# Optimization experiments

Measured on AMD Instinct MI355X. Metric: run time of the kernel, lower is better.

Reference implementation:

```python
import jax, jax.numpy as jnp
from jax import lax
import numpy as np

EPS = 1e-6
D_KQ = 256  # per-head q/k dim; softmax scale = sqrt(256) = 16


def layernorm(x, g, b):
    m = jnp.mean(x, axis=-1, keepdims=True)
    v = jnp.var(x, axis=-1, keepdims=True)  # biased, matches torch LayerNorm
    return (x - m) / jnp.sqrt(v + EPS) * g + b


def lrelu(t):
    return jnp.where(t > 0, t, 0.1 * t)


def setup_inputs() -> dict:
    key = jax.random.key(0)
    ks = jax.random.split(key, 10)
    B, C, H, W = 256, 17, 84, 84
    d_model, heads = 512, 4
    hid = D_KQ * heads  # 1024
    out_dim = 256
    s = 0.05
    return {
        "x": jax.random.normal(ks[0], (B, C, H, W), jnp.float32),
        "conv1_w": jax.random.normal(ks[1], (64, C, 8, 8), jnp.float32) * s,
        "conv1_b": jnp.zeros((64,), jnp.float32),
        "conv2_w": jax.random.normal(ks[2], (510, 64, 4, 4), jnp.float32) * s,
        "conv2_b": jnp.zeros((510,), jnp.float32),
        "wq": jax.random.normal(ks[3], (hid, d_model), jnp.float32) * s,
        "wk": jax.random.normal(ks[4], (hid, d_model), jnp.float32) * s,
        "wv": jax.random.normal(ks[5], (hid, d_model), jnp.float32) * s,
        "ln_e_g": jnp.ones((hid,), jnp.float32),
        "ln_e_b": jnp.zeros((hid,), jnp.float32),
        "wo": jax.random.normal(ks[6], (d_model, hid), jnp.float32) * s,
        "ln_g": jnp.ones((d_model,), jnp.float32),
        "ln_b": jnp.zeros((d_model,), jnp.float32),
        "map_w": jax.random.normal(ks[7], (out_dim, d_model), jnp.float32) * s,
        "map_b": jnp.zeros((out_dim,), jnp.float32),
    }


def reference(x, conv1_w, conv1_b, conv2_w, conv2_b, wq, wk, wv,
              ln_e_g, ln_e_b, wo, ln_g, ln_b, map_w, map_b):
    dn = ("NCHW", "OIHW", "NCHW")
    # feature extractor
    y = lax.conv_general_dilated(x, conv1_w, (4, 4), "VALID", dimension_numbers=dn)
    y = lrelu(y + conv1_b[None, :, None, None])
    y = lax.conv_general_dilated(y, conv2_w, (2, 2), "VALID", dimension_numbers=dn)
    y = lrelu(y + conv2_b[None, :, None, None])  # [B,510,H2,W2]
    B, Cc, H2, W2 = y.shape
    N = H2 * W2
    e = jnp.transpose(y.reshape(B, Cc, N), (0, 2, 1))  # [B,N,510]
    # coordinate augmentation: [(i//W)/H, (i%W)/W]
    idx = jnp.arange(N)
    coord = jnp.stack([(idx // W2) / H2, (idx % W2) / W2], axis=-1).astype(e.dtype)
    e = jnp.concatenate([e, jnp.broadcast_to(coord, (B, N, 2))], axis=-1)  # [B,N,512]
    heads = 4
    # projections + per-projection LayerNorm over full hid dim (pre-head-split)
    q = layernorm(e @ wq.T, ln_e_g, ln_e_b).reshape(B, N, heads, D_KQ)
    k = layernorm(e @ wk.T, ln_e_g, ln_e_b).reshape(B, N, heads, D_KQ)
    v = layernorm(e @ wv.T, ln_e_g, ln_e_b).reshape(B, N, heads, D_KQ)
    scores = jnp.einsum("bnhd,bmhd->bhnm", q, k) / jnp.sqrt(jnp.float32(D_KQ))
    w = jax.nn.softmax(scores, axis=-1)
    nv = jnp.einsum("bhnm,bmhd->bnhd", w, v).reshape(B, N, heads * D_KQ)
    out = layernorm(nv @ wo.T + e, ln_g, ln_b)  # residual + LN
    out = jax.nn.relu(out)
    out = jnp.max(out, axis=1)  # maxout over entities -> [B,512]
    return lrelu(out @ map_w.T + map_b)  # mapping -> [B,256]
```

## Files before the change

kernel.cpp:

```cpp
#include <hip/hip_runtime.h>
#include <hip/hip_bf16.h>
#include <math.h>

typedef __hip_bfloat16 bf16;
using f32x4 = __attribute__((ext_vector_type(4))) float;
using s16x8 = __attribute__((ext_vector_type(8))) short;

#define DEV_INLINE __device__ __forceinline__

static constexpr int BB   = 256;
static constexpr int CIN  = 17;
static constexpr int WIN  = 84;
static constexpr int C1   = 64;
static constexpr int W1   = 20;
static constexpr int P1   = W1 * W1;
static constexpr int C2   = 510;
static constexpr int W2   = 9;
static constexpr int NE   = 81;
static constexpr int DM   = 512;
static constexpr int HID  = 1024;
static constexpr int NH   = 4;
static constexpr int DK   = 256;
static constexpr int MR   = BB * NE;
static constexpr int ODIM = 256;
static constexpr int PLANE = WIN * WIN;
static constexpr int QS   = 3 * HID;

DEV_INLINE float lrelu_f(float v) { return v > 0.f ? v : 0.1f * v; }
DEV_INLINE float bf2f(ushort u) { return __uint_as_float((unsigned)u << 16); }
DEV_INLINE short f2bs(float f) { bf16 t = __float2bfloat16(f); return *reinterpret_cast<short*>(&t); }

DEV_INLINE void gll16(const void* g, const void* l) {
    __builtin_amdgcn_global_load_lds(
        (const __attribute__((address_space(1))) unsigned int*)g,
        (__attribute__((address_space(3))) unsigned int*)l, 16, 0, 0);
}
DEV_INLINE f32x4 mfma16(s16x8 a, s16x8 b, f32x4 c) {
    return __builtin_amdgcn_mfma_f32_16x16x32_bf16(a, b, c, 0, 0, 0);
}

__global__ void k_cast4(const float* __restrict__ s, bf16* __restrict__ d, int n4) {
    const int i4 = blockIdx.x * 256 + threadIdx.x;
    if (i4 >= n4) return;
    const size_t i = (size_t)i4 * 4;
    const float4 v = *(const float4*)(s + i);
    short o[4] = { f2bs(v.x), f2bs(v.y), f2bs(v.z), f2bs(v.w) };
    *(ushort4*)(d + i) = *(ushort4*)o;
}
__global__ void k_castw2(const float* __restrict__ s, bf16* __restrict__ d) {
    const int i = blockIdx.x * 256 + threadIdx.x;
    const int n = i >> 10, rem = i & 1023;
    const int khkw = rem >> 6, ic = rem & 63;
    d[i] = (n < C2) ? __float2bfloat16(s[n * 1024 + ic * 16 + khkw])
                    : __float2bfloat16(0.f);
}
__global__ void k_padb2(const float* __restrict__ s, float* __restrict__ d) {
    const int i = blockIdx.x * 256 + threadIdx.x;
    if (i < 512) d[i] = (i < C2) ? s[i] : 0.f;
}
__global__ void k_castqkv(const float* __restrict__ wq, const float* __restrict__ wk,
                          const float* __restrict__ wv, bf16* __restrict__ d) {
    const int i4 = blockIdx.x * 256 + threadIdx.x;
    const size_t i = (size_t)i4 * 4;
    const int n = (int)(i >> 9), c = (int)(i & 511);
    const float* src = (n < 1024) ? wq : (n < 2048) ? wk : wv;
    const int r = n & 1023;
    const float4 v = *(const float4*)(src + (size_t)r * 512 + c);
    short o[4] = { f2bs(v.x), f2bs(v.y), f2bs(v.z), f2bs(v.w) };
    *(ushort4*)(d + i) = *(ushort4*)o;
}

__global__ __launch_bounds__(512, 1) void k_conv1_mfma(const float* __restrict__ x,
        const bf16* __restrict__ w1b, const float* __restrict__ bias,
        bf16* __restrict__ y1t) {
    __shared__ __align__(16) char pl[2][28224];
    const int b = blockIdx.x;
    const int tid = threadIdx.x;
    const int w = tid >> 6, l = tid & 63;
    const int l15 = l & 15, l4 = l >> 4;
    const float* xb = x + (size_t)b * CIN * PLANE;

    int baseA[4], tval[4];
    #pragma unroll
    for (int j = 0; j < 4; ++j) {
        const int t = w + 8 * j; tval[j] = t;
        int p = t * 16 + l15; if (t >= 25) p = 0;
        const int oh = p / 20, ow = p % 20;
        baseA[j] = (oh * 4 + l4) * 336 + ow * 16;
    }
    float bias_r[4];
    #pragma unroll
    for (int nt = 0; nt < 4; ++nt) bias_r[nt] = bias[nt * 16 + l15];

    #pragma unroll
    for (int it = 0; it < 4; ++it) {
        const int g = it * 512 + tid;
        if (g < 1764) gll16(xb + (size_t)g * 4, pl[0] + (size_t)g * 16);
    }
    __syncthreads();

    f32x4 acc[4][4] = {};
    int cur = 0;
    for (int ic = 0; ic < CIN; ++ic) {
        if (ic + 1 < CIN) {
            const float* src = xb + (size_t)(ic + 1) * PLANE;
            #pragma unroll
            for (int it = 0; it < 4; ++it) {
                const int g = it * 512 + tid;
                if (g < 1764) gll16(src + (size_t)g * 4, pl[cur ^ 1] + (size_t)g * 16);
            }
        }
        s16x8 bq[4][2];
        #pragma unroll
        for (int nt = 0; nt < 4; ++nt)
            #pragma unroll
            for (int ks = 0; ks < 2; ++ks)
                bq[nt][ks] = *(const s16x8*)(w1b + (size_t)(nt * 16 + l15) * 1088
                                             + ic * 64 + (ks * 4 + l4) * 8);
        const char* P = pl[cur];
        #pragma unroll
        for (int j = 0; j < 4; ++j) {
            if (tval[j] < 25) {
                #pragma unroll
                for (int ks = 0; ks < 2; ++ks) {
                    const float* fp = (const float*)(P + baseA[j] + ks * 1344);
                    const f32x4 f0 = *(const f32x4*)fp;
                    const f32x4 f1 = *(const f32x4*)(fp + 4);
                    s16x8 af;
                    #pragma unroll
                    for (int jj = 0; jj < 4; ++jj) {
                        af[jj]     = f2bs(f0[jj]);
                        af[jj + 4] = f2bs(f1[jj]);
                    }
                    #pragma unroll
                    for (int nt = 0; nt < 4; ++nt)
                        acc[j][nt] = mfma16(af, bq[nt][ks], acc[j][nt]);
                }
            }
        }
        __syncthreads();
        cur ^= 1;
    }
    #pragma unroll
    for (int j = 0; j < 4; ++j) {
        if (tval[j] < 25) {
            #pragma unroll
            for (int nt = 0; nt < 4; ++nt) {
                #pragma unroll
                for (int q = 0; q < 4; ++q) {
                    const int pix = tval[j] * 16 + l4 * 4 + q;
                    const int oc  = nt * 16 + l15;
                    y1t[((size_t)b * P1 + pix) * 64 + oc] =
                        __float2bfloat16(lrelu_f(acc[j][nt][q] + bias_r[nt]));
                }
            }
        }
    }
}

__global__ __launch_bounds__(256) void k_gemm_conv2(const bf16* __restrict__ A,
        const bf16* __restrict__ B, const float* __restrict__ bias,
        bf16* __restrict__ Cb) {
    __shared__ __align__(16) char Asm[2][128 * 64];
    __shared__ __align__(16) char Bsm[2][128 * 64];
    const int tid = threadIdx.x;
    const int m0 = blockIdx.y * 128, n0 = blockIdx.x * 128;
    const int w = tid >> 6, l = tid & 63;
    const int wm = w >> 1, wn = w & 1;
    const int l15 = l & 15, l4 = l >> 4;
    const int r0 = tid >> 2, p0 = tid & 3;
    const int r1 = 64 + r0;
    const int sw0 = (p0 ^ ((r0 >> 1) & 3)) << 3;
    const int sw1 = (p0 ^ ((r1 >> 1) & 3)) << 3;
    int bimg[2], ohh[2], oww[2];
    #pragma unroll
    for (int it = 0; it < 2; ++it) {
        const int m = m0 + (it ? r1 : r0);
        bimg[it] = m / 81;
        const int n = m - bimg[it] * 81;
        ohh[it] = n / 9; oww[it] = n - ohh[it] * 9;
    }
    auto stage = [&](int buf, int k0) {
        const int khkw = k0 >> 6, icb = k0 & 63;
        const int kh = khkw >> 2, kwv = khkw & 3;
        const int pix0 = (ohh[0] * 2 + kh) * 20 + oww[0] * 2 + kwv;
        const int pix1 = (ohh[1] * 2 + kh) * 20 + oww[1] * 2 + kwv;
        gll16(A + ((size_t)bimg[0] * P1 + pix0) * 64 + icb + sw0, Asm[buf] + tid * 16);
        gll16(A + ((size_t)bimg[1] * P1 + pix1) * 64 + icb + sw1, Asm[buf] + (256 + tid) * 16);
        gll16(B + (size_t)(n0 + r0) * HID + k0 + sw0, Bsm[buf] + tid * 16);
        gll16(B + (size_t)(n0 + r1) * HID + k0 + sw1, Bsm[buf] + (256 + tid) * 16);
    };
    stage(0, 0);
    __syncthreads();
    f32x4 acc[4][4] = {};
    int cur = 0;
    for (int t = 0; t < 32; ++t) {
        if (t < 31) stage(cur ^ 1, (t + 1) * 32);
        s16x8 af[4], bfv[4];
        #pragma unroll
        for (int i = 0; i < 4; ++i) {
            const int ra = wm * 64 + i * 16 + l15;
            af[i]  = *(const s16x8*)(Asm[cur] + ra * 64 + ((l4 ^ ((ra >> 1) & 3)) << 4));
            const int rb = wn * 64 + i * 16 + l15;
            bfv[i] = *(const s16x8*)(Bsm[cur] + rb * 64 + ((l4 ^ ((rb >> 1) & 3)) << 4));
        }
        #pragma unroll
        for (int i = 0; i < 4; ++i)
            #pragma unroll
            for (int j = 0; j < 4; ++j)
                acc[i][j] = mfma16(af[i], bfv[j], acc[i][j]);
        __syncthreads();
        cur ^= 1;
    }
    #pragma unroll
    for (int i = 0; i < 4; ++i) {
        #pragma unroll
        for (int j = 0; j < 4; ++j) {
            const int col = n0 + wn * 64 + j * 16 + l15;
            #pragma unroll
            for (int q = 0; q < 4; ++q) {
                const int row = m0 + wm * 64 + i * 16 + l4 * 4 + q;
                float v = lrelu_f(acc[i][j][q] + bias[col]);
                if (col >= 510) {
                    const int n = row % 81;
                    v = (col == 510) ? (float)(n / 9) * (1.f / 9.f)
                                     : (float)(n % 9) * (1.f / 9.f);
                }
                Cb[(size_t)row * DM + col] = __float2bfloat16(v);
            }
        }
    }
}

template <int RESID>
__global__ __launch_bounds__(256) void k_gemm_stats(const bf16* __restrict__ A,
        const bf16* __restrict__ B, const bf16* __restrict__ resid,
        bf16* __restrict__ Cb, float2* __restrict__ part,
        int K, int ldc, int nPH) {
    __shared__ __align__(16) char Asm[2][16384];
    __shared__ __align__(16) char Bsm[2][16384];
    const int tid = threadIdx.x;
    const int m0 = blockIdx.y * 128, n0 = blockIdx.x * 128;
    const int w = tid >> 6, l = tid & 63;
    const int wm = w >> 1, wn = w & 1;
    const int l15 = l & 15, l4 = l >> 4;

    auto stage = [&](int buf, int k0) {
        #pragma unroll
        for (int it = 0; it < 4; ++it) {
            const int g = it * 256 + tid;
            const int r = g >> 3, p = g & 7;
            const int sw = (p ^ (r & 7)) << 3;
            gll16(A + (size_t)(m0 + r) * K + k0 + sw, Asm[buf] + g * 16);
            gll16(B + (size_t)(n0 + r) * K + k0 + sw, Bsm[buf] + g * 16);
        }
    };
    stage(0, 0);
    __syncthreads();
    f32x4 acc[4][4] = {};
    int cur = 0;
    const int nt = K >> 6;
    for (int t = 0; t < nt; ++t) {
        if (t + 1 < nt) stage(cur ^ 1, (t + 1) * 64);
        #pragma unroll
        for (int kk = 0; kk < 2; ++kk) {
            s16x8 af[4], bfv[4];
            const int pz = kk * 4 + l4;
            #pragma unroll
            for (int i = 0; i < 4; ++i) {
                const int ra = wm * 64 + i * 16 + l15;
                af[i]  = *(const s16x8*)(Asm[cur] + ra * 128 + ((pz ^ (ra & 7)) << 4));
                const int rb = wn * 64 + i * 16 + l15;
                bfv[i] = *(const s16x8*)(Bsm[cur] + rb * 128 + ((pz ^ (rb & 7)) << 4));
            }
            #pragma unroll
            for (int i = 0; i < 4; ++i)
                #pragma unroll
                for (int j = 0; j < 4; ++j)
                    acc[i][j] = mfma16(af[i], bfv[j], acc[i][j]);
        }
        __syncthreads();
        cur ^= 1;
    }
    #pragma unroll
    for (int i = 0; i < 4; ++i) {
        #pragma unroll
        for (int q = 0; q < 4; ++q) {
            const int row = m0 + wm * 64 + i * 16 + l4 * 4 + q;
            if (RESID) {
                const bf16* rr = resid + (size_t)row * ldc;
                #pragma unroll
                for (int j = 0; j < 4; ++j)
                    acc[i][j][q] += bf2f(*(const ushort*)(rr + n0 + wn * 64 + j * 16 + l15));
            }
            float s = 0.f, s2 = 0.f;
            #pragma unroll
            for (int j = 0; j < 4; ++j) {
                const float v = acc[i][j][q];
                s += v; s2 += v * v;
            }
            #pragma unroll
            for (int o = 1; o < 16; o <<= 1) {
                s  += __shfl_xor(s, o, 64);
                s2 += __shfl_xor(s2, o, 64);
            }
            if (l15 == 0)
                part[(size_t)row * nPH + (n0 >> 6) + wn] = make_float2(s, s2);
            bf16* cr = Cb + (size_t)row * ldc + n0 + wn * 64;
            #pragma unroll
            for (int j = 0; j < 4; ++j)
                cr[j * 16 + l15] = __float2bfloat16(acc[i][j][q]);
        }
    }
}

__global__ void k_red(const float2* __restrict__ part, float2* __restrict__ stats,
                      int total, int nPH, int groups, float invD) {
    const int gid = blockIdx.x * 256 + threadIdx.x;
    if (gid >= total) return;
    const int proj = gid / MR, row = gid - proj * MR;
    const float2* p = part + (size_t)row * (nPH * groups) + proj * nPH;
    float s = 0.f, s2 = 0.f;
    for (int h = 0; h < nPH; ++h) { s += p[h].x; s2 += p[h].y; }
    const float mean = s * invD;
    const float var  = s2 * invD - mean * mean;
    stats[gid] = make_float2(mean, rsqrtf(var + 1e-6f));
}

__global__ __launch_bounds__(256) void k_vt(const bf16* __restrict__ qkv3,
        const float2* __restrict__ vstats, const float* __restrict__ g,
        const float* __restrict__ bprm, bf16* __restrict__ vt) {
    __shared__ bf16 T[81 * 264];
    const int tid = threadIdx.x;
    const int bh = blockIdx.x;
    const int b = bh >> 2, h = bh & 3;
    const int brow = b * NE;
    const int hoff = h * DK;
    for (int gidx = tid; gidx < 81 * 32; gidx += 256) {
        const int m = gidx >> 5, c8 = gidx & 31;
        const int row = brow + m;
        const s16x8 vv = *(const s16x8*)(qkv3 + (size_t)row * QS + 2048 + hoff + c8 * 8);
        const float2 st = vstats[row];
        const int col0 = hoff + c8 * 8;
        const float4 g0 = *(const float4*)(g + col0), g1 = *(const float4*)(g + col0 + 4);
        const float4 b0 = *(const float4*)(bprm + col0), b1 = *(const float4*)(bprm + col0 + 4);
        const float ga[8] = { g0.x, g0.y, g0.z, g0.w, g1.x, g1.y, g1.z, g1.w };
        const float ba[8] = { b0.x, b0.y, b0.z, b0.w, b1.x, b1.y, b1.z, b1.w };
        short o[8];
        #pragma unroll
        for (int jj = 0; jj < 8; ++jj) {
            const float a = st.y * ga[jj];
            o[jj] = f2bs(bf2f((ushort)vv[jj]) * a + (ba[jj] - st.x * a));
        }
        *(s16x8*)(T + m * 264 + c8 * 8) = *(s16x8*)o;
    }
    __syncthreads();
    const int d = tid;
    bf16 row[96];
    #pragma unroll
    for (int m = 0; m < 81; ++m) row[m] = T[m * 264 + d];
    #pragma unroll
    for (int m = 81; m < 96; ++m) row[m] = __float2bfloat16(0.f);
    bf16* out = vt + ((size_t)bh * DK + d) * 96;
    #pragma unroll
    for (int g8 = 0; g8 < 12; ++g8)
        *(s16x8*)(out + g8 * 8) = *(const s16x8*)(&row[g8 * 8]);
}

__global__ __launch_bounds__(512) void k_attn3(const bf16* __restrict__ qkv3,
        const float2* __restrict__ stats, const float* __restrict__ g,
        const float* __restrict__ bprm, const bf16* __restrict__ vt,
        bf16* __restrict__ nv) {
    __shared__ __align__(16) char smem[49152 + 96 * 104 * 2];
    char* Ks = smem;
    bf16* Pb = (bf16*)(smem + 49152);
    const int tid = threadIdx.x;
    const int bh = blockIdx.x;
    const int b = bh >> 2, h = bh & 3;
    const int brow = b * NE;
    const int hoff = h * DK;
    const int w = tid >> 6, l = tid & 63;
    const int l15 = l & 15, l4 = l >> 4;

    for (int gidx = tid; gidx < 96 * 32; gidx += 512) {
        const int r = gidx >> 5, c8 = gidx & 31;
        int krow = brow + r; if (krow >= MR) krow = MR - 1;
        const s16x8 kv = *(const s16x8*)(qkv3 + (size_t)krow * QS + 1024 + hoff + c8 * 8);
        const float2 st = stats[MR + krow];
        const int col0 = hoff + c8 * 8;
        const float4 g0 = *(const float4*)(g + col0), g1 = *(const float4*)(g + col0 + 4);
        const float4 b0 = *(const float4*)(bprm + col0), b1 = *(const float4*)(bprm + col0 + 4);
        const float ga[8] = { g0.x, g0.y, g0.z, g0.w, g1.x, g1.y, g1.z, g1.w };
        const float ba[8] = { b0.x, b0.y, b0.z, b0.w, b1.x, b1.y, b1.z, b1.w };
        short o[8];
        #pragma unroll
        for (int jj = 0; jj < 8; ++jj) {
            const float a = st.y * ga[jj];
            o[jj] = f2bs(bf2f((ushort)kv[jj]) * a + (ba[jj] - st.x * a));
        }
        *(s16x8*)(Ks + r * 512 + ((c8 ^ (r & 7)) << 4)) = *(s16x8*)o;
    }
    __syncthreads();

    if (w < 6) {
        int qrow = brow + w * 16 + l15; if (qrow >= MR) qrow = MR - 1;
        const float2 stq = stats[qrow];
        s16x8 qa[8];
        #pragma unroll
        for (int kk = 0; kk < 8; ++kk) {
            const int col0 = hoff + kk * 32 + l4 * 8;
            const s16x8 qv = *(const s16x8*)(qkv3 + (size_t)qrow * QS + col0);
            const float4 g0 = *(const float4*)(g + col0), g1 = *(const float4*)(g + col0 + 4);
            const float4 b0 = *(const float4*)(bprm + col0), b1 = *(const float4*)(bprm + col0 + 4);
            const float ga[8] = { g0.x, g0.y, g0.z, g0.w, g1.x, g1.y, g1.z, g1.w };
            const float ba[8] = { b0.x, b0.y, b0.z, b0.w, b1.x, b1.y, b1.z, b1.w };
            short o[8];
            #pragma unroll
            for (int jj = 0; jj < 8; ++jj) {
                const float a = stq.y * ga[jj];
                o[jj] = f2bs(bf2f((ushort)qv[jj]) * a + (ba[jj] - stq.x * a));
            }
            qa[kk] = *(s16x8*)o;
        }
        f32x4 sacc[6];
        #pragma unroll
        for (int j = 0; j < 6; ++j) {
            f32x4 a = {};
            const int rb = j * 16 + l15;
            #pragma unroll
            for (int kk = 0; kk < 8; ++kk) {
                const s16x8 kf = *(const s16x8*)(Ks + rb * 512 + (((kk * 4 + l4) ^ (rb & 7)) << 4));
                a = mfma16(qa[kk], kf, a);
            }
            sacc[j] = a;
        }
        float px[6][4];
        #pragma unroll
        for (int q = 0; q < 4; ++q) {
            float m = -1e30f;
            #pragma unroll
            for (int j = 0; j < 6; ++j) {
                const int key = j * 16 + l15;
                const float v = (key < NE) ? sacc[j][q] : -1e30f;
                px[j][q] = v;
                m = fmaxf(m, v);
            }
            #pragma unroll
            for (int o = 1; o < 16; o <<= 1) m = fmaxf(m, __shfl_xor(m, o, 64));
            float s = 0.f;
            #pragma unroll
            for (int j = 0; j < 6; ++j) {
                const float e = __expf((px[j][q] - m) * 0.0625f);
                px[j][q] = e; s += e;
            }
            #pragma unroll
            for (int o = 1; o < 16; o <<= 1) s += __shfl_xor(s, o, 64);
            const float r = 1.f / s;
            #pragma unroll
            for (int j = 0; j < 6; ++j) px[j][q] *= r;
        }
        #pragma unroll
        for (int j = 0; j < 6; ++j)
            #pragma unroll
            for (int q = 0; q < 4; ++q)
                Pb[(w * 16 + l4 * 4 + q) * 104 + j * 16 + l15] =
                    __float2bfloat16(px[j][q]);
    }
    __syncthreads();

    const bf16* vtb = vt + (size_t)bh * DK * 96;
    s16x8 vf[2][3];
    #pragma unroll
    for (int dj = 0; dj < 2; ++dj) {
        const int d = (2 * w + dj) * 16 + l15;
        #pragma unroll
        for (int ks = 0; ks < 3; ++ks)
            vf[dj][ks] = *(const s16x8*)(vtb + (size_t)d * 96 + (ks * 4 + l4) * 8);
    }
    f32x4 oacc[6][2] = {};
    #pragma unroll
    for (int i = 0; i < 6; ++i) {
        s16x8 pa[3];
        #pragma unroll
        for (int ks = 0; ks < 3; ++ks)
            pa[ks] = *(const s16x8*)(Pb + (i * 16 + l15) * 104 + (ks * 4 + l4) * 8);
        #pragma unroll
        for (int dj = 0; dj < 2; ++dj)
            #pragma unroll
            for (int ks = 0; ks < 3; ++ks)
                oacc[i][dj] = mfma16(pa[ks], vf[dj][ks], oacc[i][dj]);
    }
    #pragma unroll
    for (int i = 0; i < 6; ++i) {
        #pragma unroll
        for (int q = 0; q < 4; ++q) {
            const int n = i * 16 + l4 * 4 + q;
            if (n < NE) {
                #pragma unroll
                for (int dj = 0; dj < 2; ++dj) {
                    const int d = (2 * w + dj) * 16 + l15;
                    nv[(size_t)(brow + n) * HID + hoff + d] =
                        __float2bfloat16(oacc[i][dj][q]);
                }
            }
        }
    }
}

__global__ void k_maxpool_ln(const bf16* __restrict__ X, const float2* __restrict__ st,
        const float* __restrict__ g, const float* __restrict__ bprm,
        float* __restrict__ P) {
    const int i = blockIdx.x * 256 + threadIdx.x;
    const int bb = i >> 9, c = i & 511;
    const float gc = g[c], bc = bprm[c];
    const bf16* xp = X + (size_t)bb * NE * DM + c;
    const float2* sp = st + (size_t)bb * NE;
    float mx = -1e30f;
    for (int n = 0; n < NE; ++n) {
        const float2 s = sp[n];
        const float a = s.y * gc;
        const float v = __bfloat162float(xp[(size_t)n * DM]) * a + (bc - s.x * a);
        mx = fmaxf(mx, fmaxf(v, 0.f));
    }
    P[i] = mx;
}

__global__ __launch_bounds__(256) void k_final(const float* __restrict__ P,
        const float* __restrict__ W, const float* __restrict__ bias,
        float* __restrict__ out) {
    const int bb = blockIdx.x;
    __shared__ float pr[DM];
    for (int i = threadIdx.x; i < DM; i += 256) pr[i] = P[(size_t)bb * DM + i];
    __syncthreads();
    const int o = threadIdx.x;
    const float4* w4 = (const float4*)(W + (size_t)o * DM);
    float acc = 0.f;
    for (int c4 = 0; c4 < DM / 4; ++c4) {
        const float4 wv = w4[c4];
        acc += wv.x * pr[c4 * 4] + wv.y * pr[c4 * 4 + 1]
             + wv.z * pr[c4 * 4 + 2] + wv.w * pr[c4 * 4 + 3];
    }
    out[(size_t)bb * ODIM + o] = lrelu_f(acc + bias[o]);
}

extern "C" void kernel_launch(void* const* d_in, const int* in_sizes, int n_in,
                              void* d_out, int out_size, void* d_ws, size_t ws_size,
                              hipStream_t stream) {
    const float* x   = (const float*)d_in[0];
    const float* w1  = (const float*)d_in[1];
    const float* b1  = (const float*)d_in[2];
    const float* w2  = (const float*)d_in[3];
    const float* b2  = (const float*)d_in[4];
    const float* wq  = (const float*)d_in[5];
    const float* wk  = (const float*)d_in[6];
    const float* wvv = (const float*)d_in[7];
    const float* lng = (const float*)d_in[8];
    const float* lnb = (const float*)d_in[9];
    const float* wo  = (const float*)d_in[10];
    const float* lg2 = (const float*)d_in[11];
    const float* lb2 = (const float*)d_in[12];
    const float* mw  = (const float*)d_in[13];
    const float* mb  = (const float*)d_in[14];

    char* ws = (char*)d_ws;
    size_t off = 0;
    auto alloc = [&](size_t bytes) {
        void* p = ws + off;
        off = (off + bytes + 255) & ~(size_t)255;
        return p;
    };
    bf16*   y1t   = (bf16*)  alloc((size_t)BB * P1 * 64 * 2);
    bf16*   ebf   = (bf16*)  alloc((size_t)MR * DM * 2);
    bf16*   qkv3  = (bf16*)  alloc((size_t)MR * QS * 2);
    bf16*   vt    = (bf16*)  alloc((size_t)BB * NH * DK * 96 * 2);
    bf16*   nv    = (bf16*)  alloc((size_t)MR * HID * 2);
    bf16*   ao    = (bf16*)  alloc((size_t)MR * DM * 2);
    float*  pool  = (float*) alloc((size_t)BB * DM * 4);
    float2* part1 = (float2*)alloc((size_t)MR * 48 * 8);
    float2* part2 = (float2*)alloc((size_t)MR * 8 * 8);
    float2* stQKV = (float2*)alloc((size_t)3 * MR * 8);
    float2* st2   = (float2*)alloc((size_t)MR * 8);
    bf16*   w1b   = (bf16*)  alloc((size_t)C1 * CIN * 64 * 2);
    bf16*   w2b   = (bf16*)  alloc((size_t)512 * HID * 2);
    float*  b2p   = (float*) alloc(512 * 4);
    bf16*   wqkv  = (bf16*)  alloc((size_t)3072 * DM * 2);
    bf16*   wob   = (bf16*)  alloc((size_t)DM * HID * 2);
    float*  outp  = (float*)d_out;

    k_cast4<<<(C1 * CIN * 64 / 4 + 255) / 256, 256, 0, stream>>>(w1, w1b, C1 * CIN * 64 / 4);
    k_castw2<<<512 * HID / 256, 256, 0, stream>>>(w2, w2b);
    k_padb2<<<2, 256, 0, stream>>>(b2, b2p);
    k_castqkv<<<3072 * DM / 4 / 256, 256, 0, stream>>>(wq, wk, wvv, wqkv);
    k_cast4<<<(DM * HID / 4) / 256, 256, 0, stream>>>(wo, wob, DM * HID / 4);

    k_conv1_mfma<<<BB, 512, 0, stream>>>(x, w1b, b1, y1t);

    k_gemm_conv2<<<dim3(4, MR / 128), 256, 0, stream>>>(y1t, w2b, b2p, ebf);

    k_gemm_stats<0><<<dim3(24, MR / 128), 256, 0, stream>>>(ebf, wqkv, nullptr,
                                                            qkv3, part1, DM, QS, 48);
    k_red<<<(3 * MR + 255) / 256, 256, 0, stream>>>(part1, stQKV, 3 * MR, 16, 3,
                                                    1.f / 1024.f);

    k_vt<<<BB * NH, 256, 0, stream>>>(qkv3, stQKV + 2 * MR, lng, lnb, vt);

    k_attn3<<<BB * NH, 512, 0, stream>>>(qkv3, stQKV, lng, lnb, vt, nv);

    k_gemm_stats<1><<<dim3(4, MR / 128), 256, 0, stream>>>(nv, wob, ebf,
                                                           ao, part2, HID, DM, 8);
    k_red<<<(MR + 255) / 256, 256, 0, stream>>>(part2, st2, MR, 8, 1, 1.f / 512.f);

    k_maxpool_ln<<<(BB * DM) / 256, 256, 0, stream>>>(ao, st2, lg2, lb2, pool);
    k_final<<<BB, 256, 0, stream>>>(pool, mw, mb, outp);
}
```

Baseline: 390.2 us.

## Replace QKV projection GEMM with 256x256-tile 8-wave pipelined kernel

Swaps the 128x128-tile k_gemm_stats launch for the QKV projection with a dedicated kernel that uses 256x256 tiles, 8 waves, and 128KB of LDS. Global-to-LDS loads are staggered across four compute phases with explicit vmcnt waits, barriers and raised s_setprio around the MFMA bursts. The aim is more data reuse per tile and better overlap of memory traffic with matrix math. In exchange, the grid has fewer blocks, register pressure is high with 128 accumulator floats per lane, and the hand-tuned wait counts are fragile.

```diff
diff --git a/kernel.cpp b/kernel.cpp
--- a/kernel.cpp
+++ b/kernel.cpp
@@ -228,6 +228,119 @@
                 }
                 Cb[(size_t)row * DM + col] = __float2bfloat16(v);
             }
+        }
+    }
+}
+
+#define QKV_PHASE(QD, STAGING, TAIL)                                           \
+    {                                                                          \
+        s16x8 areg[2][2];                                                      \
+        _Pragma("unroll")                                                      \
+        for (int ii = 0; ii < 2; ++ii) {                                       \
+            const int fr = QD * 32 + ii * 16 + l15;                            \
+            _Pragma("unroll")                                                  \
+            for (int kk = 0; kk < 2; ++kk)                                     \
+                areg[ii][kk] = *(const s16x8*)(Abase + fr * 128 +              \
+                                   (((kk * 4 + l4) ^ (fr & 7)) << 4));         \
+        }                                                                      \
+        STAGING;                                                               \
+        __builtin_amdgcn_s_barrier();                                          \
+        asm volatile("s_waitcnt lgkmcnt(0)" ::: "memory");                     \
+        __builtin_amdgcn_sched_barrier(0);                                     \
+        __builtin_amdgcn_s_setprio(1);                                         \
+        _Pragma("unroll")                                                      \
+        for (int ii = 0; ii < 2; ++ii)                                         \
+            _Pragma("unroll")                                                  \
+            for (int j = 0; j < 4; ++j)                                        \
+                _Pragma("unroll")                                              \
+                for (int kk = 0; kk < 2; ++kk)                                 \
+                    acc[QD * 2 + ii][j] =                                      \
+                        mfma16(areg[ii][kk], breg[j][kk], acc[QD * 2 + ii][j]);\
+        __builtin_amdgcn_s_setprio(0);                                         \
+        TAIL;                                                                  \
+        __builtin_amdgcn_s_barrier();                                          \
+        __builtin_amdgcn_sched_barrier(0);                                     \
+    }
+
+__global__ __launch_bounds__(512, 2) void k_gemm_qkv8(const bf16* __restrict__ A,
+        const bf16* __restrict__ B, bf16* __restrict__ Cb,
+        float2* __restrict__ part) {
+    __shared__ __align__(16) char lds[131072];
+    const int tid = threadIdx.x;
+    const int m0 = blockIdx.y * 256, n0 = blockIdx.x * 256;
+    const int wid = tid >> 6, l = tid & 63;
+    const int wm = wid >> 2, wn = wid & 3;
+    const int l15 = l & 15, l4 = l >> 4;
+    const int rA = tid >> 3, pA = tid & 7;
+
+    auto stageA = [&](int buf, int kt, int qa) {
+        char* dst = lds + buf * 32768 + (qa >> 1) * 16384 + (qa & 1) * 8192 + tid * 16;
+        gll16(A + (size_t)(m0 + qa * 64 + rA) * 512 + kt * 64 + ((pA ^ (rA & 7)) << 3), dst);
+    };
+    auto stageB = [&](int buf, int kt, int hb) {
+        char* base = lds + 65536 + buf * 32768 + hb * 16384;
+        #pragma unroll
+        for (int i2 = 0; i2 < 2; ++i2) {
+            const int s = i2 * 512 + tid;
+            const int c = s >> 3, pp = s & 7;
+            gll16(B + (size_t)(n0 + hb * 128 + c) * 512 + kt * 64 + ((pp ^ (c & 7)) << 3),
+                  base + s * 16);
+        }
+    };
+
+    stageA(0, 0, 0); stageA(0, 0, 1); stageA(0, 0, 2); stageA(0, 0, 3);
+    stageB(0, 0, 0); stageB(0, 0, 1);
+    stageB(1, 1, 0); stageB(1, 1, 1);
+    stageA(1, 1, 0); stageA(1, 1, 2);
+    asm volatile("s_waitcnt vmcnt(6)" ::: "memory");
+    __builtin_amdgcn_s_barrier();
+    __builtin_amdgcn_sched_barrier(0);
+
+    f32x4 acc[8][4] = {};
+    for (int kt = 0; kt < 8; ++kt) {
+        const int cur = kt & 1;
+        const char* Abase = lds + cur * 32768 + wm * 16384;
+        const char* Bbase = lds + 65536 + cur * 32768 + (wn >> 1) * 16384;
+        s16x8 breg[4][2];
+        #pragma unroll
+        for (int j = 0; j < 4; ++j) {
+            const int fc = (wn & 1) * 64 + j * 16 + l15;
+            #pragma unroll
+            for (int kk = 0; kk < 2; ++kk)
+                breg[j][kk] = *(const s16x8*)(Bbase + fc * 128 +
+                                  (((kk * 4 + l4) ^ (fc & 7)) << 4));
+        }
+        QKV_PHASE(0, { if (kt + 1 < 8) { stageA(cur ^ 1, kt + 1, 1); stageA(cur ^ 1, kt + 1, 3); } }, {})
+        QKV_PHASE(1, { if (kt + 2 < 8) { stageB(cur, kt + 2, 0); } }, {})
+        QKV_PHASE(2, { if (kt + 2 < 8) { stageB(cur, kt + 2, 1); stageA(cur, kt + 2, 0); stageA(cur, kt + 2, 2); } }, {})
+        QKV_PHASE(3, { }, {
+            if (kt < 6)       { asm volatile("s_waitcnt vmcnt(6)" ::: "memory"); }
+            else if (kt == 6) { asm volatile("s_waitcnt vmcnt(0)" ::: "memory"); }
+        })
+    }
+
+    #pragma unroll
+    for (int fi = 0; fi < 8; ++fi) {
+        #pragma unroll
+        for (int q = 0; q < 4; ++q) {
+            const int row = m0 + wm * 128 + fi * 16 + l4 * 4 + q;
+            float s = 0.f, s2 = 0.f;
+            #pragma unroll
+            for (int j = 0; j < 4; ++j) {
+                const float v = acc[fi][j][q];
+                s += v; s2 += v * v;
+            }
+            #pragma unroll
+            for (int o = 1; o < 16; o <<= 1) {
+                s  += __shfl_xor(s, o, 64);
+                s2 += __shfl_xor(s2, o, 64);
+            }
+            if (l15 == 0)
+                part[(size_t)row * 48 + blockIdx.x * 4 + wn] = make_float2(s, s2);
+            bf16* cr = Cb + (size_t)row * QS + n0 + wn * 64;
+            #pragma unroll
+            for (int j = 0; j < 4; ++j)
+                cr[j * 16 + l15] = __float2bfloat16(acc[fi][j][q]);
         }
     }
 }
@@ -597,8 +710,7 @@
 
     k_gemm_conv2<<<dim3(4, MR / 128), 256, 0, stream>>>(y1t, w2b, b2p, ebf);
 
-    k_gemm_stats<0><<<dim3(24, MR / 128), 256, 0, stream>>>(ebf, wqkv, nullptr,
-                                                            qkv3, part1, DM, QS, 48);
+    k_gemm_qkv8<<<dim3(12, MR / 256), 512, 0, stream>>>(ebf, wqkv, qkv3, part1);
     k_red<<<(3 * MR + 255) / 256, 256, 0, stream>>>(part1, stQKV, 3 * MR, 16, 3,
                                                     1.f / 1024.f);
 
```

After: 371.1 us. 4.9% less time.
